# Kernel optimization log

Hardware: AMD Instinct MI355X
Metric: run time of the kernel (lower is better)

Reference implementation:

```python
import jax, jax.numpy as jnp
import numpy as np

N = 32768      # input points
P = 16         # num_points (kernel points == max neighbors per center)
NC = 8192      # centers after fps(ratio=0.25)
E = NC * P     # edges (exactly P neighbors per center, grouped by center)
IN_F = 64
OUT_F = 128
RADIUS = 1.0
KP_EXTENT = RADIUS / 1.5


def setup_inputs() -> dict:
    key = jax.random.key(0)
    k1, k2, k3, k4, k5 = jax.random.split(key, 5)
    x = jax.random.normal(k1, (N, IN_F), dtype=jnp.float32)
    pos = jax.random.normal(k2, (N, 3), dtype=jnp.float32)
    edge_src = jax.random.randint(k3, (E,), 0, N, dtype=jnp.int32)
    # edges grouped contiguously per center, P edges each (radius() output layout)
    edge_tgt = (jnp.arange(E, dtype=jnp.int32) // P)
    # kernel point positions inside the ball of radius KP-layout scale
    kernel_pts = jax.random.uniform(k4, (P, 3), dtype=jnp.float32,
                                    minval=-0.66 * RADIUS, maxval=0.66 * RADIUS)
    # kaiming-uniform-like init for [P, in, out] per-kernel-point weights
    bound = 1.0 / np.sqrt(IN_F)
    kernel_weight = jax.random.uniform(k5, (P, IN_F, OUT_F), dtype=jnp.float32,
                                       minval=-bound, maxval=bound)
    return {"x": x, "pos": pos, "edge_src": edge_src, "edge_tgt": edge_tgt,
            "kernel_pts": kernel_pts, "kernel_weight": kernel_weight}


def reference(x, pos, edge_src, edge_tgt, kernel_pts, kernel_weight):
    n_edges = edge_src.shape[0]
    nc = n_edges // P
    # gather endpoints (message_x_and_pos: pos_i, pos_j, x_j)
    pos_i = pos[edge_tgt]                       # [E,3]
    pos_j = pos[edge_src]                       # [E,3]
    rel = (pos_i - pos_j).reshape(nc, P, 3)     # neighbors, [NC,P,3]
    # distances from every neighbor to every kernel point
    diff = rel[:, :, None, :] - kernel_pts[None, None, :, :]   # [NC,P,K,3]
    sq = jnp.sum(diff * diff, axis=-1)                          # [NC,P,K]
    # linear KP influence, clamped at 0
    all_w = jnp.maximum(1.0 - jnp.sqrt(sq) / KP_EXTENT, 0.0)
    # one-hot argmin kernel assignment (VQ-like selection)
    nn_idx = jnp.argmin(sq, axis=-1)                            # [NC,P]
    one_hot = jax.nn.one_hot(nn_idx, P, dtype=all_w.dtype)      # [NC,P,K]
    all_w = all_w * one_hot
    feat = x[edge_src].reshape(nc, P, IN_F)                     # [NC,P,in]
    # weighted_features = all_w @ feat  (contract kernel axis vs neighbor axis)
    wf = jnp.einsum('cnk,cki->cni', all_w, feat)                # [NC,P,in]
    # per-edge matmul with the argmin-selected weight matrix; one_hot selects
    # W[nn_idx] without materializing the [E,in,out] gather
    msg = jnp.einsum('cni,cnk,kio->cno', wf, one_hot, kernel_weight)  # [NC,P,out]
    # scatter-add aggregation over target centers (MessagePassing aggr='add')
    out = jax.ops.segment_sum(msg.reshape(-1, OUT_F), edge_tgt, num_segments=NC)
    return out
```

## Files before the change

kernel.cpp:

```cpp
#include <hip/hip_runtime.h>
#include <hip/hip_bf16.h>


#define P 16
#define IN_F 64
#define OUT_F 128
#define NCC 8192
#define KPE 0.6666667f

typedef short short8 __attribute__((ext_vector_type(8)));
typedef float floatx4 __attribute__((ext_vector_type(4)));

__device__ inline unsigned short f2bf(float f) {
    __hip_bfloat16 h = __float2bfloat16(f);
    return __builtin_bit_cast(unsigned short, h);
}

__global__ __launch_bounds__(256) void kconv_w(const float* __restrict__ Wf,
                                               unsigned short* __restrict__ Wb) {
    int tg = blockIdx.x * 256 + threadIdx.x;
    int m = tg >> 13;
    int n = (tg >> 6) & 127;
    int i = tg & 63;
    Wb[tg] = f2bf(Wf[(m * 64 + i) * 128 + n]);
}

__global__ __launch_bounds__(512) void kconv_main(
    const float* __restrict__ x, const float* __restrict__ pos,
    const int* __restrict__ esrc, const int* __restrict__ etgt,
    const float* __restrict__ kpts, const unsigned short* __restrict__ Wb,
    float* __restrict__ out)
{
    __shared__ float kps[48];
    __shared__ float wv[512];
    __shared__ int   nnv[512];
    __shared__ int   srcv[512];
    __shared__ float s_loc[512];
    __shared__ __align__(16) unsigned short As[32 * 72];
    __shared__ __align__(16) unsigned short Bs[128 * 72];

    const int t  = threadIdx.x;
    const int c0 = blockIdx.x * 32;

    if (t < 48) kps[t] = kpts[t];

    const int e   = c0 * P + t;
    const int src = esrc[e];
    const int tgt = etgt[e];
    float rx = __fsub_rn(pos[tgt * 3 + 0], pos[src * 3 + 0]);
    float ry = __fsub_rn(pos[tgt * 3 + 1], pos[src * 3 + 1]);
    float rz = __fsub_rn(pos[tgt * 3 + 2], pos[src * 3 + 2]);
    __syncthreads();
    float best = 1e30f; int nn = 0;
#pragma unroll
    for (int k = 0; k < 16; ++k) {
        float dx = __fsub_rn(rx, kps[k * 3 + 0]);
        float dy = __fsub_rn(ry, kps[k * 3 + 1]);
        float dz = __fsub_rn(rz, kps[k * 3 + 2]);
        float sq = __fadd_rn(__fadd_rn(__fmul_rn(dx, dx), __fmul_rn(dy, dy)),
                             __fmul_rn(dz, dz));
        if (sq < best) { best = sq; nn = k; }
    }
    float w = fmaxf(__fsub_rn(1.0f, __fdiv_rn(__fsqrt_rn(best), KPE)), 0.0f);
    wv[t] = w; nnv[t] = nn; srcv[t] = src;
    __syncthreads();

    {
        int cl = t >> 4, mm = t & 15;
        float sacc = 0.f;
#pragma unroll
        for (int n2 = 0; n2 < 16; ++n2) {
            int idx = cl * 16 + n2;
            sacc += (nnv[idx] == mm) ? wv[idx] : 0.f;
        }
        s_loc[t] = sacc;
    }
    __syncthreads();

    const float4* x4 = reinterpret_cast<const float4*>(x);
    const uint4*  wb4 = reinterpret_cast<const uint4*>(Wb);
    const int ar = t >> 4, aq = t & 15;
    const int bn = t >> 3, bsg = t & 7;
    const int bn2 = (t + 512) >> 3, bsg2 = (t + 512) & 7;

    const int wave = t >> 6, lane = t & 63;
    const int quad = lane >> 4, l16 = lane & 15;
    const int rgi = wave & 1, cgi = wave >> 1;
    const int aoff  = (rgi * 16 + l16) * 72;
    const int boff0 = (cgi * 32 + l16) * 72;
    const int boff1 = (cgi * 32 + 16 + l16) * 72;
    const int koff  = quad * 8;

    floatx4 acc0 = {0.f, 0.f, 0.f, 0.f};
    floatx4 acc1 = {0.f, 0.f, 0.f, 0.f};

    float4 xv = x4[srcv[ar * 16 + 0] * 16 + aq];
    uint4 bv0 = wb4[t];
    uint4 bv1 = wb4[t + 512];

    for (int m = 0; m < 16; ++m) {
        float sv = s_loc[ar * 16 + m];
        ushort4 av;
        av.x = f2bf(sv * xv.x); av.y = f2bf(sv * xv.y);
        av.z = f2bf(sv * xv.z); av.w = f2bf(sv * xv.w);
        *reinterpret_cast<ushort4*>(&As[ar * 72 + aq * 4]) = av;
        *reinterpret_cast<uint4*>(&Bs[bn  * 72 + bsg  * 8]) = bv0;
        *reinterpret_cast<uint4*>(&Bs[bn2 * 72 + bsg2 * 8]) = bv1;
        __syncthreads();

        if (m < 15) {
            xv  = x4[srcv[ar * 16 + m + 1] * 16 + aq];
            bv0 = wb4[(m + 1) * 1024 + t];
            bv1 = wb4[(m + 1) * 1024 + t + 512];
        }

#pragma unroll
        for (int ks = 0; ks < 2; ++ks) {
            short8 a  = *reinterpret_cast<const short8*>(&As[aoff  + ks * 32 + koff]);
            short8 b0 = *reinterpret_cast<const short8*>(&Bs[boff0 + ks * 32 + koff]);
            acc0 = __builtin_amdgcn_mfma_f32_16x16x32_bf16(a, b0, acc0, 0, 0, 0);
            short8 b1 = *reinterpret_cast<const short8*>(&Bs[boff1 + ks * 32 + koff]);
            acc1 = __builtin_amdgcn_mfma_f32_16x16x32_bf16(a, b1, acc1, 0, 0, 0);
        }
        __syncthreads();
    }

    const int colbase = cgi * 32 + l16;
    const int rowbase = c0 + rgi * 16 + quad * 4;
#pragma unroll
    for (int v = 0; v < 4; ++v) {
        out[(rowbase + v) * 128 + colbase]      = acc0[v];
        out[(rowbase + v) * 128 + colbase + 16] = acc1[v];
    }
}

extern "C" void kernel_launch(void* const* d_in, const int* in_sizes, int n_in,
                              void* d_out, int out_size, void* d_ws, size_t ws_size,
                              hipStream_t stream) {
    const float* x    = (const float*)d_in[0];
    const float* pos  = (const float*)d_in[1];
    const int*   esrc = (const int*)d_in[2];
    const int*   etgt = (const int*)d_in[3];
    const float* kpts = (const float*)d_in[4];
    const float* Wf   = (const float*)d_in[5];
    float* out = (float*)d_out;
    unsigned short* Wb = (unsigned short*)d_ws;

    hipLaunchKernelGGL(kconv_w, dim3(512), dim3(256), 0, stream, Wf, Wb);
    hipLaunchKernelGGL(kconv_main, dim3(NCC / 32), dim3(512), 0, stream,
                       x, pos, esrc, etgt, kpts, Wb, out);
}
```

Measured before the change: 83.20 us.

## Halve block tile to 16 centers and double-buffer LDS with two-stage prefetch

Each block now processes 16 centers with 256 threads instead of 32 centers with 512, which doubles the grid size. The A and B LDS tiles are double-buffered, and global loads of x and the bf16 weights are prefetched two stages ahead. This removes one barrier per iteration and overlaps MFMA work with staging of the next tile. In exchange, each block reloads the full weight slice for half as many rows, so per-center weight traffic doubles and register pressure rises from the prefetch buffers.

```diff
diff --git a/kernel.cpp b/kernel.cpp
--- a/kernel.cpp
+++ b/kernel.cpp
@@ -25,26 +25,26 @@
     Wb[tg] = f2bf(Wf[(m * 64 + i) * 128 + n]);
 }
 
-__global__ __launch_bounds__(512) void kconv_main(
+__global__ __launch_bounds__(256) void kconv_main(
     const float* __restrict__ x, const float* __restrict__ pos,
     const int* __restrict__ esrc, const int* __restrict__ etgt,
     const float* __restrict__ kpts, const unsigned short* __restrict__ Wb,
     float* __restrict__ out)
 {
     __shared__ float kps[48];
-    __shared__ float wv[512];
-    __shared__ int   nnv[512];
-    __shared__ int   srcv[512];
-    __shared__ float s_loc[512];
-    __shared__ __align__(16) unsigned short As[32 * 72];
-    __shared__ __align__(16) unsigned short Bs[128 * 72];
+    __shared__ float wv[256];
+    __shared__ int   nnv[256];
+    __shared__ int   srcv[256];
+    __shared__ float s_loc[256];
+    __shared__ __align__(16) unsigned short As[2][16 * 72];
+    __shared__ __align__(16) unsigned short Bs[2][128 * 72];
 
-    const int t  = threadIdx.x;
-    const int c0 = blockIdx.x * 32;
+    const int t   = threadIdx.x;
+    const int c0  = blockIdx.x * 16;
 
     if (t < 48) kps[t] = kpts[t];
 
-    const int e   = c0 * P + t;
+    const int e   = blockIdx.x * 256 + t;
     const int src = esrc[e];
     const int tgt = etgt[e];
     float rx = __fsub_rn(pos[tgt * 3 + 0], pos[src * 3 + 0]);
@@ -75,62 +75,86 @@
         }
         s_loc[t] = sacc;
     }
+
+    const float4* x4  = reinterpret_cast<const float4*>(x);
+    const uint4*  wb4 = reinterpret_cast<const uint4*>(Wb);
+    const int ar = t >> 4, aq = t & 15;
+    const int ar16 = ar * 16;
+
+    float4 xa[2];
+    uint4  bv[2][4];
+    xa[0] = x4[srcv[ar16 + 0] * 16 + aq];
+    xa[1] = x4[srcv[ar16 + 1] * 16 + aq];
+#pragma unroll
+    for (int j = 0; j < 4; ++j) {
+        bv[0][j] = wb4[0 * 1024 + j * 256 + t];
+        bv[1][j] = wb4[1 * 1024 + j * 256 + t];
+    }
     __syncthreads();
 
-    const float4* x4 = reinterpret_cast<const float4*>(x);
-    const uint4*  wb4 = reinterpret_cast<const uint4*>(Wb);
-    const int ar = t >> 4, aq = t & 15;
-    const int bn = t >> 3, bsg = t & 7;
-    const int bn2 = (t + 512) >> 3, bsg2 = (t + 512) & 7;
+    {
+        float sv = s_loc[ar16 + 0];
+        ushort4 av;
+        av.x = f2bf(sv * xa[0].x); av.y = f2bf(sv * xa[0].y);
+        av.z = f2bf(sv * xa[0].z); av.w = f2bf(sv * xa[0].w);
+        *reinterpret_cast<ushort4*>(&As[0][ar * 72 + aq * 4]) = av;
+#pragma unroll
+        for (int j = 0; j < 4; ++j) {
+            int u = j * 256 + t;
+            *reinterpret_cast<uint4*>(&Bs[0][(u >> 3) * 72 + (u & 7) * 8]) = bv[0][j];
+        }
+    }
 
     const int wave = t >> 6, lane = t & 63;
     const int quad = lane >> 4, l16 = lane & 15;
-    const int rgi = wave & 1, cgi = wave >> 1;
-    const int aoff  = (rgi * 16 + l16) * 72;
-    const int boff0 = (cgi * 32 + l16) * 72;
-    const int boff1 = (cgi * 32 + 16 + l16) * 72;
+    const int aoff  = l16 * 72;
+    const int boff0 = ((wave * 2 + 0) * 16 + l16) * 72;
+    const int boff1 = ((wave * 2 + 1) * 16 + l16) * 72;
     const int koff  = quad * 8;
 
     floatx4 acc0 = {0.f, 0.f, 0.f, 0.f};
     floatx4 acc1 = {0.f, 0.f, 0.f, 0.f};
 
-    float4 xv = x4[srcv[ar * 16 + 0] * 16 + aq];
-    uint4 bv0 = wb4[t];
-    uint4 bv1 = wb4[t + 512];
-
+#pragma unroll
     for (int m = 0; m < 16; ++m) {
-        float sv = s_loc[ar * 16 + m];
-        ushort4 av;
-        av.x = f2bf(sv * xv.x); av.y = f2bf(sv * xv.y);
-        av.z = f2bf(sv * xv.z); av.w = f2bf(sv * xv.w);
-        *reinterpret_cast<ushort4*>(&As[ar * 72 + aq * 4]) = av;
-        *reinterpret_cast<uint4*>(&Bs[bn  * 72 + bsg  * 8]) = bv0;
-        *reinterpret_cast<uint4*>(&Bs[bn2 * 72 + bsg2 * 8]) = bv1;
+        const int cur = m & 1, nxt = 1 - cur;
         __syncthreads();
-
-        if (m < 15) {
-            xv  = x4[srcv[ar * 16 + m + 1] * 16 + aq];
-            bv0 = wb4[(m + 1) * 1024 + t];
-            bv1 = wb4[(m + 1) * 1024 + t + 512];
-        }
 
 #pragma unroll
         for (int ks = 0; ks < 2; ++ks) {
-            short8 a  = *reinterpret_cast<const short8*>(&As[aoff  + ks * 32 + koff]);
-            short8 b0 = *reinterpret_cast<const short8*>(&Bs[boff0 + ks * 32 + koff]);
+            short8 a  = *reinterpret_cast<const short8*>(&As[cur][aoff  + ks * 32 + koff]);
+            short8 b0 = *reinterpret_cast<const short8*>(&Bs[cur][boff0 + ks * 32 + koff]);
             acc0 = __builtin_amdgcn_mfma_f32_16x16x32_bf16(a, b0, acc0, 0, 0, 0);
-            short8 b1 = *reinterpret_cast<const short8*>(&Bs[boff1 + ks * 32 + koff]);
+            short8 b1 = *reinterpret_cast<const short8*>(&Bs[cur][boff1 + ks * 32 + koff]);
             acc1 = __builtin_amdgcn_mfma_f32_16x16x32_bf16(a, b1, acc1, 0, 0, 0);
         }
-        __syncthreads();
+
+        if (m < 15) {
+            float sv = s_loc[ar16 + m + 1];
+            ushort4 av;
+            av.x = f2bf(sv * xa[nxt].x); av.y = f2bf(sv * xa[nxt].y);
+            av.z = f2bf(sv * xa[nxt].z); av.w = f2bf(sv * xa[nxt].w);
+            *reinterpret_cast<ushort4*>(&As[nxt][ar * 72 + aq * 4]) = av;
+#pragma unroll
+            for (int j = 0; j < 4; ++j) {
+                int u = j * 256 + t;
+                *reinterpret_cast<uint4*>(&Bs[nxt][(u >> 3) * 72 + (u & 7) * 8]) = bv[nxt][j];
+            }
+            if (m < 14) {
+                xa[cur] = x4[srcv[ar16 + m + 2] * 16 + aq];
+#pragma unroll
+                for (int j = 0; j < 4; ++j)
+                    bv[cur][j] = wb4[(m + 2) * 1024 + j * 256 + t];
+            }
+        }
     }
 
-    const int colbase = cgi * 32 + l16;
-    const int rowbase = c0 + rgi * 16 + quad * 4;
+    const int col  = wave * 32 + l16;
+    const int row0 = c0 + quad * 4;
 #pragma unroll
     for (int v = 0; v < 4; ++v) {
-        out[(rowbase + v) * 128 + colbase]      = acc0[v];
-        out[(rowbase + v) * 128 + colbase + 16] = acc1[v];
+        out[(row0 + v) * 128 + col]      = acc0[v];
+        out[(row0 + v) * 128 + col + 16] = acc1[v];
     }
 }
 
@@ -147,6 +171,6 @@
     unsigned short* Wb = (unsigned short*)d_ws;
 
     hipLaunchKernelGGL(kconv_w, dim3(512), dim3(256), 0, stream, Wf, Wb);
-    hipLaunchKernelGGL(kconv_main, dim3(NCC / 32), dim3(512), 0, stream,
+    hipLaunchKernelGGL(kconv_main, dim3(NCC / 16), dim3(256), 0, stream,
                        x, pos, esrc, etgt, kpts, Wb, out);
 }
```

Result: slower. 107.3 us (+29.0%).

## Pre-convert x to bf16 and feed MFMA from registers with post-MMA scaling

Applied to the files above, without the earlier changes.

A prep kernel now converts x to bf16 along with the weights, and the weight transpose goes through shared memory so reads are coalesced. The main kernel no longer stages A and B tiles in LDS. Each wave loads bf16 x rows and W fragments directly into registers with double buffering, runs the MFMA into a temporary accumulator, and applies the per-row influence scale afterwards, so the per-iteration barriers go away. In exchange, x is rounded to bf16 before scaling rather than after, and each wave issues more redundant global or L2 loads of W.

```diff
diff --git a/kernel.cpp b/kernel.cpp
--- a/kernel.cpp
+++ b/kernel.cpp
@@ -2,10 +2,6 @@
 #include <hip/hip_bf16.h>
 
 
-#define P 16
-#define IN_F 64
-#define OUT_F 128
-#define NCC 8192
 #define KPE 0.6666667f
 
 typedef short short8 __attribute__((ext_vector_type(8)));
@@ -16,35 +12,50 @@
     return __builtin_bit_cast(unsigned short, h);
 }
 
-__global__ __launch_bounds__(256) void kconv_w(const float* __restrict__ Wf,
-                                               unsigned short* __restrict__ Wb) {
-    int tg = blockIdx.x * 256 + threadIdx.x;
-    int m = tg >> 13;
-    int n = (tg >> 6) & 127;
-    int i = tg & 63;
-    Wb[tg] = f2bf(Wf[(m * 64 + i) * 128 + n]);
+__global__ __launch_bounds__(256) void kconv_prep(const float* __restrict__ Wf,
+                                                  const float* __restrict__ x,
+                                                  unsigned short* __restrict__ Wb,
+                                                  unsigned short* __restrict__ xb) {
+    const int t = threadIdx.x;
+    if (blockIdx.x < 16) {
+        const int m = blockIdx.x;
+        __shared__ float tile[64 * 129];
+#pragma unroll
+        for (int j = 0; j < 32; ++j) {
+            int idx = j * 256 + t;
+            tile[(idx >> 7) * 129 + (idx & 127)] = Wf[m * 8192 + idx];
+        }
+        __syncthreads();
+#pragma unroll
+        for (int j = 0; j < 32; ++j) {
+            int idx = j * 256 + t;
+            Wb[m * 8192 + idx] = f2bf(tile[(idx & 63) * 129 + (idx >> 6)]);
+        }
+    } else {
+        int idx4 = (blockIdx.x - 16) * 256 + t;
+        const float4 v = reinterpret_cast<const float4*>(x)[idx4];
+        ushort4 o;
+        o.x = f2bf(v.x); o.y = f2bf(v.y); o.z = f2bf(v.z); o.w = f2bf(v.w);
+        reinterpret_cast<ushort4*>(xb)[idx4] = o;
+    }
 }
 
 __global__ __launch_bounds__(512) void kconv_main(
-    const float* __restrict__ x, const float* __restrict__ pos,
+    const unsigned short* __restrict__ xb, const float* __restrict__ pos,
     const int* __restrict__ esrc, const int* __restrict__ etgt,
     const float* __restrict__ kpts, const unsigned short* __restrict__ Wb,
     float* __restrict__ out)
 {
     __shared__ float kps[48];
-    __shared__ float wv[512];
-    __shared__ int   nnv[512];
-    __shared__ int   srcv[512];
-    __shared__ float s_loc[512];
-    __shared__ __align__(16) unsigned short As[32 * 72];
-    __shared__ __align__(16) unsigned short Bs[128 * 72];
+    __shared__ float wv[32 * 17];
+    __shared__ int   nnv[32 * 17];
+    __shared__ int   srcv[16 * 32];
+    __shared__ __align__(16) float s_loc[16 * 32];
 
-    const int t  = threadIdx.x;
-    const int c0 = blockIdx.x * 32;
-
+    const int t = threadIdx.x;
     if (t < 48) kps[t] = kpts[t];
 
-    const int e   = c0 * P + t;
+    const int e   = blockIdx.x * 512 + t;
     const int src = esrc[e];
     const int tgt = etgt[e];
     float rx = __fsub_rn(pos[tgt * 3 + 0], pos[src * 3 + 0]);
@@ -62,75 +73,90 @@
         if (sq < best) { best = sq; nn = k; }
     }
     float w = fmaxf(__fsub_rn(1.0f, __fdiv_rn(__fsqrt_rn(best), KPE)), 0.0f);
-    wv[t] = w; nnv[t] = nn; srcv[t] = src;
+    {
+        const int r = t >> 4, n = t & 15;
+        wv[r * 17 + n] = w; nnv[r * 17 + n] = nn;
+        srcv[n * 32 + r] = src;
+    }
     __syncthreads();
 
     {
-        int cl = t >> 4, mm = t & 15;
+        const int m = t >> 5, rr = t & 31;
         float sacc = 0.f;
 #pragma unroll
-        for (int n2 = 0; n2 < 16; ++n2) {
-            int idx = cl * 16 + n2;
-            sacc += (nnv[idx] == mm) ? wv[idx] : 0.f;
-        }
-        s_loc[t] = sacc;
+        for (int n2 = 0; n2 < 16; ++n2)
+            sacc += (nnv[rr * 17 + n2] == m) ? wv[rr * 17 + n2] : 0.f;
+        s_loc[m * 32 + rr] = sacc;
     }
     __syncthreads();
 
-    const float4* x4 = reinterpret_cast<const float4*>(x);
-    const uint4*  wb4 = reinterpret_cast<const uint4*>(Wb);
-    const int ar = t >> 4, aq = t & 15;
-    const int bn = t >> 3, bsg = t & 7;
-    const int bn2 = (t + 512) >> 3, bsg2 = (t + 512) & 7;
+    const uint4* xb4 = reinterpret_cast<const uint4*>(xb);
+    const uint4* wb4 = reinterpret_cast<const uint4*>(Wb);
+    const int wave = t >> 6, lane = t & 63;
+    const int rg = wave & 1, cq = wave >> 2 ? (wave >> 1) & 3 : (wave >> 1) & 3;
+    const int l16 = lane & 15, quad = lane >> 4;
+    const int cqq = wave >> 1;
+    const int arow = rg * 16 + l16;
+    const int bq0 = (cqq * 32 + l16) * 8 + quad;
+    const int bq1 = bq0 + 16 * 8;
+    const int svoff = rg * 16 + quad * 4;
 
-    const int wave = t >> 6, lane = t & 63;
-    const int quad = lane >> 4, l16 = lane & 15;
-    const int rgi = wave & 1, cgi = wave >> 1;
-    const int aoff  = (rgi * 16 + l16) * 72;
-    const int boff0 = (cgi * 32 + l16) * 72;
-    const int boff1 = (cgi * 32 + 16 + l16) * 72;
-    const int koff  = quad * 8;
+    uint4 A[2][2], B[2][4];
+    float4 SV[2];
+    {
+        int s0 = srcv[arow];
+        A[0][0] = xb4[s0 * 8 + quad];
+        A[0][1] = xb4[s0 * 8 + 4 + quad];
+        B[0][0] = wb4[bq0];
+        B[0][1] = wb4[bq0 + 4];
+        B[0][2] = wb4[bq1];
+        B[0][3] = wb4[bq1 + 4];
+        SV[0] = *reinterpret_cast<const float4*>(&s_loc[svoff]);
+    }
 
     floatx4 acc0 = {0.f, 0.f, 0.f, 0.f};
     floatx4 acc1 = {0.f, 0.f, 0.f, 0.f};
-
-    float4 xv = x4[srcv[ar * 16 + 0] * 16 + aq];
-    uint4 bv0 = wb4[t];
-    uint4 bv1 = wb4[t + 512];
-
-    for (int m = 0; m < 16; ++m) {
-        float sv = s_loc[ar * 16 + m];
-        ushort4 av;
-        av.x = f2bf(sv * xv.x); av.y = f2bf(sv * xv.y);
-        av.z = f2bf(sv * xv.z); av.w = f2bf(sv * xv.w);
-        *reinterpret_cast<ushort4*>(&As[ar * 72 + aq * 4]) = av;
-        *reinterpret_cast<uint4*>(&Bs[bn  * 72 + bsg  * 8]) = bv0;
-        *reinterpret_cast<uint4*>(&Bs[bn2 * 72 + bsg2 * 8]) = bv1;
-        __syncthreads();
-
-        if (m < 15) {
-            xv  = x4[srcv[ar * 16 + m + 1] * 16 + aq];
-            bv0 = wb4[(m + 1) * 1024 + t];
-            bv1 = wb4[(m + 1) * 1024 + t + 512];
-        }
+    const floatx4 zed = {0.f, 0.f, 0.f, 0.f};
 
 #pragma unroll
-        for (int ks = 0; ks < 2; ++ks) {
-            short8 a  = *reinterpret_cast<const short8*>(&As[aoff  + ks * 32 + koff]);
-            short8 b0 = *reinterpret_cast<const short8*>(&Bs[boff0 + ks * 32 + koff]);
-            acc0 = __builtin_amdgcn_mfma_f32_16x16x32_bf16(a, b0, acc0, 0, 0, 0);
-            short8 b1 = *reinterpret_cast<const short8*>(&Bs[boff1 + ks * 32 + koff]);
-            acc1 = __builtin_amdgcn_mfma_f32_16x16x32_bf16(a, b1, acc1, 0, 0, 0);
+    for (int m = 0; m < 16; ++m) {
+        const int cur = m & 1, nxt = cur ^ 1;
+        if (m < 15) {
+            int sn = srcv[(m + 1) * 32 + arow];
+            A[nxt][0] = xb4[sn * 8 + quad];
+            A[nxt][1] = xb4[sn * 8 + 4 + quad];
+            const int wb = (m + 1) * 1024;
+            B[nxt][0] = wb4[wb + bq0];
+            B[nxt][1] = wb4[wb + bq0 + 4];
+            B[nxt][2] = wb4[wb + bq1];
+            B[nxt][3] = wb4[wb + bq1 + 4];
+            SV[nxt] = *reinterpret_cast<const float4*>(&s_loc[(m + 1) * 32 + svoff]);
         }
-        __syncthreads();
+        short8 a0 = __builtin_bit_cast(short8, A[cur][0]);
+        short8 a1 = __builtin_bit_cast(short8, A[cur][1]);
+        floatx4 t0 = __builtin_amdgcn_mfma_f32_16x16x32_bf16(
+            a0, __builtin_bit_cast(short8, B[cur][0]), zed, 0, 0, 0);
+        t0 = __builtin_amdgcn_mfma_f32_16x16x32_bf16(
+            a1, __builtin_bit_cast(short8, B[cur][1]), t0, 0, 0, 0);
+        floatx4 t1 = __builtin_amdgcn_mfma_f32_16x16x32_bf16(
+            a0, __builtin_bit_cast(short8, B[cur][2]), zed, 0, 0, 0);
+        t1 = __builtin_amdgcn_mfma_f32_16x16x32_bf16(
+            a1, __builtin_bit_cast(short8, B[cur][3]), t1, 0, 0, 0);
+        const float4 sv = SV[cur];
+#pragma unroll
+        for (int v = 0; v < 4; ++v) {
+            const float s4 = (v == 0) ? sv.x : (v == 1) ? sv.y : (v == 2) ? sv.z : sv.w;
+            acc0[v] += s4 * t0[v];
+            acc1[v] += s4 * t1[v];
+        }
     }
 
-    const int colbase = cgi * 32 + l16;
-    const int rowbase = c0 + rgi * 16 + quad * 4;
+    const int col  = cqq * 32 + l16;
+    const int row0 = blockIdx.x * 32 + rg * 16 + quad * 4;
 #pragma unroll
     for (int v = 0; v < 4; ++v) {
-        out[(rowbase + v) * 128 + colbase]      = acc0[v];
-        out[(rowbase + v) * 128 + colbase + 16] = acc1[v];
+        out[(row0 + v) * 128 + col]      = acc0[v];
+        out[(row0 + v) * 128 + col + 16] = acc1[v];
     }
 }
 
@@ -144,9 +170,13 @@
     const float* kpts = (const float*)d_in[4];
     const float* Wf   = (const float*)d_in[5];
     float* out = (float*)d_out;
-    unsigned short* Wb = (unsigned short*)d_ws;
 
-    hipLaunchKernelGGL(kconv_w, dim3(512), dim3(256), 0, stream, Wf, Wb);
-    hipLaunchKernelGGL(kconv_main, dim3(NCC / 32), dim3(512), 0, stream,
-                       x, pos, esrc, etgt, kpts, Wb, out);
+    char* wsb = (char*)d_ws;
+    unsigned short* Wb = (unsigned short*)wsb;
+    unsigned short* xb = (unsigned short*)(wsb + 262144);
+
+    hipLaunchKernelGGL(kconv_prep, dim3(16 + 2048), dim3(256), 0, stream,
+                       Wf, x, Wb, xb);
+    hipLaunchKernelGGL(kconv_main, dim3(256), dim3(512), 0, stream,
+                       xb, pos, esrc, etgt, kpts, Wb, out);
 }
```

After: 96.75 us. 16.3% more time.
